# Kernel tuning notes

Measured on AMD Instinct MI355X. Metric: run time of the kernel, lower is better.

The kernel has to match this reference:

```python
import jax, jax.numpy as jnp
import numpy as np

NUM_GROUPS = 50   # hardcoded in convert_groupandcate_to_one_hot
ALPHA = 2.0       # forward() default
MARGIN = 0.8      # forward() default


def setup_inputs() -> dict:
    key = jax.random.key(0)
    k1, k2, k3, k4 = jax.random.split(key, 4)
    B, C, N = 4, 64, 4096
    l0_points = jax.random.normal(k1, (B, N, 3), dtype=jnp.float32)
    Fsim = jax.random.normal(k2, (B, C, N), dtype=jnp.float32)
    target = jax.random.randint(k3, (B, N), 0, NUM_GROUPS, dtype=jnp.int32)
    # sprinkle some -1 (ungrouped) labels, matching real SGPN data
    drop = jax.random.uniform(k4, (B, N)) < 0.02
    target = jnp.where(drop, jnp.int32(-1), target)
    return {"l0_points": l0_points, "Fsim": Fsim, "target": target}


def reference(l0_points, Fsim, target):
    B, C, N = Fsim.shape
    # pairwise squared-distance Gram matrix: D[i,j] = |f_i|^2 + |f_j|^2 - 2<f_i,f_j>
    r = jnp.sum(Fsim * Fsim, axis=1)                      # [B, N]
    gram = jnp.einsum('bcn,bcm->bnm', Fsim, Fsim)          # [B, N, N]
    D = jnp.maximum(r[:, :, None] + r[:, None, :] - 2.0 * gram, 0.0)

    # one-hot group labels; label -1 contributes all-zeros row
    valid = (target != -1)
    one_hot = (jax.nn.one_hot(jnp.where(valid, target, 0), NUM_GROUPS,
                              dtype=jnp.float32)
               * valid[..., None].astype(jnp.float32))     # [B, N, G]

    same = jnp.einsum('bng,bmg->bnm', one_hot, one_hot)    # same-group indicator
    eye = jnp.eye(N, dtype=same.dtype)
    same = same * (1.0 - eye) + eye                        # diagonal forced to 1
    diff = 1.0 - same

    pos = same * D
    neg = ALPHA * diff * jnp.maximum(MARGIN - D, 0.0)

    # NOTE: original returns grouplabels (not the count weights) as group_mask,
    # so the weight is the outer product of the raw integer labels.
    tf = target.astype(jnp.float32)
    w = tf[:, :, None] * tf[:, None, :]                    # [B, N, N]

    return jnp.mean((pos + neg) * w)
```

## Files before the change

kernel.cpp:

```cpp
#include <hip/hip_runtime.h>
#include <hip/hip_bf16.h>
#include <stdint.h>


#define NT 32
#define TRI 528
#define NPAIR (4*TRI)
#define NBLK 512
#define SCALE (1.0f/67108864.0f)

typedef __attribute__((ext_vector_type(4))) float f32x4;
typedef __attribute__((ext_vector_type(8))) __bf16 bf16x8;

__device__ __forceinline__ void async_load16(const void* g, void* l) {
    __builtin_amdgcn_global_load_lds(
        (const __attribute__((address_space(1))) uint32_t*)g,
        (__attribute__((address_space(3))) uint32_t*)l,
        16, 0, 0);
}

__global__ __launch_bounds__(256) void sgpn_prep(
    const float* __restrict__ Fsim, const int* __restrict__ target,
    unsigned short* __restrict__ gA, float* __restrict__ gR,
    float* __restrict__ gK, float* __restrict__ gW)
{
    __shared__ float sPart[4][64];

    int blk = blockIdx.x;
    int b = blk >> 6;
    int n0 = (blk & 63) * 64;
    int lane = threadIdx.x & 63;
    int wave = threadIdx.x >> 6;

    int n = n0 + lane;
    int gp = b * 4096 + n;
    const float* src = Fsim + (size_t)b * 64 * 4096 + n;
    int tile = n >> 7, row = n & 127;
    unsigned short* dst = gA + (size_t)(b * NT + tile) * 8192 + row * 8;

    float racc = 0.f;
    #pragma unroll
    for (int q = 0; q < 2; ++q) {
        int chunk = wave * 2 + q;
        unsigned us[8];
        #pragma unroll
        for (int j = 0; j < 8; ++j) {
            float f = src[(size_t)(chunk * 8 + j) * 4096];
            unsigned u = __float_as_uint(f);
            u += 0x7fffu + ((u >> 16) & 1u);
            us[j] = u >> 16;
            float fb = __uint_as_float(us[j] << 16);
            racc = fmaf(fb, fb, racc);
        }
        uint4 pk;
        pk.x = us[0] | (us[1] << 16);
        pk.y = us[2] | (us[3] << 16);
        pk.z = us[4] | (us[5] << 16);
        pk.w = us[6] | (us[7] << 16);
        *(uint4*)(dst + chunk * 1024) = pk;
    }
    sPart[wave][lane] = racc;
    __syncthreads();
    if (wave == 0) {
        gR[gp] = (sPart[0][lane] + sPart[1][lane]) +
                 (sPart[2][lane] + sPart[3][lane]);
        int tg = target[gp];
        gK[gp] = (tg >= 0) ? (float)tg : -(float)(n + 2);
        gW[gp] = (float)tg;
    }
}

__global__ __launch_bounds__(256, 2) void sgpn_main(
    const unsigned short* __restrict__ gA,
    const float* __restrict__ gR, const float* __restrict__ gK,
    const float* __restrict__ gW, float* __restrict__ gP)
{
    __shared__ __align__(16) unsigned short lT[2][2][8192];
    __shared__ __align__(16) float sM[2][2][3][128];
    __shared__ float sRed[4];
    __shared__ float sMult[2];

    int tid = threadIdx.x;
    int lane = tid & 63;
    int wave = tid >> 6;
    int g = blockIdx.x;
    int np = (g < (NPAIR - 4 * NBLK)) ? 5 : 4;

    auto stage = [&](int P, int buf) {
        int b = P / TRI;
        int t = P - b * TRI;
        int tj = (int)((sqrtf(8.0f * (float)t + 1.0f) - 1.0f) * 0.5f);
        while ((tj + 1) * (tj + 2) / 2 <= t) ++tj;
        while (tj * (tj + 1) / 2 > t) --tj;
        int ti = t - tj * (tj + 1) / 2;

        const unsigned short* tA = gA + (size_t)(b * NT + ti) * 8192;
        const unsigned short* tB = gA + (size_t)(b * NT + tj) * 8192;
        #pragma unroll
        for (int it = 0; it < 4; ++it) {
            int e = it * 256 + tid;
            async_load16(tA + e * 8, &lT[buf][0][e * 8]);
            async_load16(tB + e * 8, &lT[buf][1][e * 8]);
        }
        int half = tid >> 7, p0 = tid & 127;
        int gp = b * 4096 + (half ? tj : ti) * 128 + p0;
        sM[buf][half][0][p0] = gR[gp];
        sM[buf][half][1][p0] = gK[gp];
        sM[buf][half][2][p0] = gW[gp];
        if (tid == 0) sMult[buf] = (ti == tj) ? 1.f : 2.f;
    };

    int wr = wave >> 1, wc = wave & 1;
    int quad = lane >> 4, lcol = lane & 15;

    float total = 0.f;
    stage(g, 0);

    for (int q = 0; q < np; ++q) {
        __syncthreads();
        int buf = q & 1;
        if (q + 1 < np) stage(g + (q + 1) * NBLK, buf ^ 1);

        f32x4 acc[4][4];
        #pragma unroll
        for (int i = 0; i < 4; ++i)
            #pragma unroll
            for (int j = 0; j < 4; ++j)
                acc[i][j] = (f32x4)0.f;

        #pragma unroll
        for (int kb = 0; kb < 2; ++kb) {
            int chunk = kb * 4 + quad;
            bf16x8 fa[4], fb[4];
            #pragma unroll
            for (int i = 0; i < 4; ++i)
                fa[i] = *(const bf16x8*)&lT[buf][0][chunk * 1024 + (wr * 64 + i * 16 + lcol) * 8];
            #pragma unroll
            for (int j = 0; j < 4; ++j)
                fb[j] = *(const bf16x8*)&lT[buf][1][chunk * 1024 + (wc * 64 + j * 16 + lcol) * 8];
            #pragma unroll
            for (int i = 0; i < 4; ++i)
                #pragma unroll
                for (int j = 0; j < 4; ++j)
                    acc[i][j] = __builtin_amdgcn_mfma_f32_16x16x32_bf16(fa[i], fb[j], acc[i][j], 0, 0, 0);
        }

        float rcv[4], kcv[4], wcv[4];
        #pragma unroll
        for (int j = 0; j < 4; ++j) {
            int cl = wc * 64 + j * 16 + lcol;
            rcv[j] = sM[buf][1][0][cl];
            kcv[j] = sM[buf][1][1][cl];
            wcv[j] = sM[buf][1][2][cl];
        }

        float sum = 0.f;
        #pragma unroll
        for (int i = 0; i < 4; ++i) {
            int rb = wr * 64 + i * 16 + quad * 4;
            f32x4 rr4 = *(const f32x4*)&sM[buf][0][0][rb];
            f32x4 kr4 = *(const f32x4*)&sM[buf][0][1][rb];
            f32x4 wr4 = *(const f32x4*)&sM[buf][0][2][rb];
            #pragma unroll
            for (int r = 0; r < 4; ++r) {
                float rrow = rr4[r], krow = kr4[r], wrow = wr4[r];
                float psum = 0.f;
                #pragma unroll
                for (int j = 0; j < 4; ++j) {
                    float gacc = acc[i][j][r];
                    float d0 = fmaf(-2.f, gacc, rrow + rcv[j]);
                    float D  = fmaxf(d0, 0.f);
                    float h  = fmaxf(fmaf(D, -2.f, 1.6f), 0.f);
                    float v  = (krow == kcv[j]) ? D : h;
                    psum = fmaf(v, wcv[j], psum);
                }
                sum = fmaf(psum, wrow, sum);
            }
        }
        total = fmaf(sum, sMult[buf], total);
    }

    #pragma unroll
    for (int off = 32; off > 0; off >>= 1)
        total += __shfl_down(total, off, 64);
    if (lane == 0) sRed[wave] = total;
    __syncthreads();
    if (tid == 0)
        gP[g] = (sRed[0] + sRed[1]) + (sRed[2] + sRed[3]);
}

__global__ __launch_bounds__(256) void sgpn_reduce(
    const float* __restrict__ gP, float* __restrict__ out)
{
    __shared__ float sr[4];
    int tid = threadIdx.x;
    float s = gP[tid] + gP[tid + 256];
    #pragma unroll
    for (int off = 32; off > 0; off >>= 1)
        s += __shfl_down(s, off, 64);
    if ((tid & 63) == 0) sr[tid >> 6] = s;
    __syncthreads();
    if (tid == 0)
        out[0] = ((sr[0] + sr[1]) + (sr[2] + sr[3])) * SCALE;
}

extern "C" void kernel_launch(void* const* d_in, const int* in_sizes, int n_in,
                              void* d_out, int out_size, void* d_ws, size_t ws_size,
                              hipStream_t stream) {
    const float* Fsim  = (const float*)d_in[1];
    const int* target  = (const int*)d_in[2];
    float* out = (float*)d_out;

    char* ws = (char*)d_ws;
    unsigned short* gA = (unsigned short*)ws;
    float* gR = (float*)(ws + (2u << 20));
    float* gK = (float*)(ws + (2u << 20) + (64u << 10));
    float* gW = (float*)(ws + (2u << 20) + (128u << 10));
    float* gP = (float*)(ws + (2u << 20) + (192u << 10));

    sgpn_prep<<<256, 256, 0, stream>>>(Fsim, target, gA, gR, gK, gW);
    sgpn_main<<<NBLK, 256, 0, stream>>>(gA, gR, gK, gW, gP);
    sgpn_reduce<<<1, 256, 0, stream>>>(gP, out);
}
```

Before: 77.30 us.

## Fuse prep, main and reduce kernels into one cooperative launch with grid syncs

```diff
diff --git a/kernel.cpp b/kernel.cpp
--- a/kernel.cpp
+++ b/kernel.cpp
@@ -1,4 +1,5 @@
 #include <hip/hip_runtime.h>
+#include <hip/hip_cooperative_groups.h>
 #include <hip/hip_bf16.h>
 #include <stdint.h>
 
@@ -12,6 +13,8 @@
 typedef __attribute__((ext_vector_type(4))) float f32x4;
 typedef __attribute__((ext_vector_type(8))) __bf16 bf16x8;
 
+namespace cg = cooperative_groups;
+
 __device__ __forceinline__ void async_load16(const void* g, void* l) {
     __builtin_amdgcn_global_load_lds(
         (const __attribute__((address_space(1))) uint32_t*)g,
@@ -19,71 +22,67 @@
         16, 0, 0);
 }
 
-__global__ __launch_bounds__(256) void sgpn_prep(
+__global__ __launch_bounds__(256, 2) void sgpn_fused(
     const float* __restrict__ Fsim, const int* __restrict__ target,
     unsigned short* __restrict__ gA, float* __restrict__ gR,
-    float* __restrict__ gK, float* __restrict__ gW)
-{
-    __shared__ float sPart[4][64];
-
-    int blk = blockIdx.x;
-    int b = blk >> 6;
-    int n0 = (blk & 63) * 64;
-    int lane = threadIdx.x & 63;
-    int wave = threadIdx.x >> 6;
-
-    int n = n0 + lane;
-    int gp = b * 4096 + n;
-    const float* src = Fsim + (size_t)b * 64 * 4096 + n;
-    int tile = n >> 7, row = n & 127;
-    unsigned short* dst = gA + (size_t)(b * NT + tile) * 8192 + row * 8;
-
-    float racc = 0.f;
-    #pragma unroll
-    for (int q = 0; q < 2; ++q) {
-        int chunk = wave * 2 + q;
-        unsigned us[8];
-        #pragma unroll
-        for (int j = 0; j < 8; ++j) {
-            float f = src[(size_t)(chunk * 8 + j) * 4096];
-            unsigned u = __float_as_uint(f);
-            u += 0x7fffu + ((u >> 16) & 1u);
-            us[j] = u >> 16;
-            float fb = __uint_as_float(us[j] << 16);
-            racc = fmaf(fb, fb, racc);
-        }
-        uint4 pk;
-        pk.x = us[0] | (us[1] << 16);
-        pk.y = us[2] | (us[3] << 16);
-        pk.z = us[4] | (us[5] << 16);
-        pk.w = us[6] | (us[7] << 16);
-        *(uint4*)(dst + chunk * 1024) = pk;
-    }
-    sPart[wave][lane] = racc;
-    __syncthreads();
-    if (wave == 0) {
-        gR[gp] = (sPart[0][lane] + sPart[1][lane]) +
-                 (sPart[2][lane] + sPart[3][lane]);
-        int tg = target[gp];
-        gK[gp] = (tg >= 0) ? (float)tg : -(float)(n + 2);
-        gW[gp] = (float)tg;
-    }
-}
-
-__global__ __launch_bounds__(256, 2) void sgpn_main(
-    const unsigned short* __restrict__ gA,
-    const float* __restrict__ gR, const float* __restrict__ gK,
-    const float* __restrict__ gW, float* __restrict__ gP)
+    float* __restrict__ gK, float* __restrict__ gW,
+    float* __restrict__ gP, float* __restrict__ out)
 {
     __shared__ __align__(16) unsigned short lT[2][2][8192];
     __shared__ __align__(16) float sM[2][2][3][128];
     __shared__ float sRed[4];
     __shared__ float sMult[2];
+    __shared__ float sPart[4][64];
 
     int tid = threadIdx.x;
     int lane = tid & 63;
     int wave = tid >> 6;
     int g = blockIdx.x;
+
+    if (g < 256) {
+        int b = g >> 6;
+        int n0 = (g & 63) * 64;
+
+        int n = n0 + lane;
+        int gp = b * 4096 + n;
+        const float* src = Fsim + (size_t)b * 64 * 4096 + n;
+        int tile = n >> 7, row = n & 127;
+        unsigned short* dst = gA + (size_t)(b * NT + tile) * 8192 + row * 8;
+
+        float racc = 0.f;
+        #pragma unroll
+        for (int q = 0; q < 2; ++q) {
+            int chunk = wave * 2 + q;
+            unsigned us[8];
+            #pragma unroll
+            for (int j = 0; j < 8; ++j) {
+                float f = src[(size_t)(chunk * 8 + j) * 4096];
+                unsigned u = __float_as_uint(f);
+                u += 0x7fffu + ((u >> 16) & 1u);
+                us[j] = u >> 16;
+                float fb = __uint_as_float(us[j] << 16);
+                racc = fmaf(fb, fb, racc);
+            }
+            uint4 pk;
+            pk.x = us[0] | (us[1] << 16);
+            pk.y = us[2] | (us[3] << 16);
+            pk.z = us[4] | (us[5] << 16);
+            pk.w = us[6] | (us[7] << 16);
+            *(uint4*)(dst + chunk * 1024) = pk;
+        }
+        sPart[wave][lane] = racc;
+        __syncthreads();
+        if (wave == 0) {
+            gR[gp] = (sPart[0][lane] + sPart[1][lane]) +
+                     (sPart[2][lane] + sPart[3][lane]);
+            int tg = target[gp];
+            gK[gp] = (tg >= 0) ? (float)tg : -(float)(n + 2);
+            gW[gp] = (float)tg;
+        }
+    }
+    __threadfence();
+    cg::this_grid().sync();
+
     int np = (g < (NPAIR - 4 * NBLK)) ? 5 : 4;
 
     auto stage = [&](int P, int buf) {
@@ -187,6 +186,190 @@
     __syncthreads();
     if (tid == 0)
         gP[g] = (sRed[0] + sRed[1]) + (sRed[2] + sRed[3]);
+
+    __threadfence();
+    cg::this_grid().sync();
+
+    if (g == 0) {
+        float s = gP[tid] + gP[tid + 256];
+        #pragma unroll
+        for (int off = 32; off > 0; off >>= 1)
+            s += __shfl_down(s, off, 64);
+        if ((tid & 63) == 0) sRed[tid >> 6] = s;
+        __syncthreads();
+        if (tid == 0)
+            out[0] = ((sRed[0] + sRed[1]) + (sRed[2] + sRed[3])) * SCALE;
+    }
+}
+
+__global__ __launch_bounds__(256) void sgpn_prep(
+    const float* __restrict__ Fsim, const int* __restrict__ target,
+    unsigned short* __restrict__ gA, float* __restrict__ gR,
+    float* __restrict__ gK, float* __restrict__ gW)
+{
+    __shared__ float sPart[4][64];
+
+    int blk = blockIdx.x;
+    int b = blk >> 6;
+    int n0 = (blk & 63) * 64;
+    int lane = threadIdx.x & 63;
+    int wave = threadIdx.x >> 6;
+
+    int n = n0 + lane;
+    int gp = b * 4096 + n;
+    const float* src = Fsim + (size_t)b * 64 * 4096 + n;
+    int tile = n >> 7, row = n & 127;
+    unsigned short* dst = gA + (size_t)(b * NT + tile) * 8192 + row * 8;
+
+    float racc = 0.f;
+    #pragma unroll
+    for (int q = 0; q < 2; ++q) {
+        int chunk = wave * 2 + q;
+        unsigned us[8];
+        #pragma unroll
+        for (int j = 0; j < 8; ++j) {
+            float f = src[(size_t)(chunk * 8 + j) * 4096];
+            unsigned u = __float_as_uint(f);
+            u += 0x7fffu + ((u >> 16) & 1u);
+            us[j] = u >> 16;
+            float fb = __uint_as_float(us[j] << 16);
+            racc = fmaf(fb, fb, racc);
+        }
+        uint4 pk;
+        pk.x = us[0] | (us[1] << 16);
+        pk.y = us[2] | (us[3] << 16);
+        pk.z = us[4] | (us[5] << 16);
+        pk.w = us[6] | (us[7] << 16);
+        *(uint4*)(dst + chunk * 1024) = pk;
+    }
+    sPart[wave][lane] = racc;
+    __syncthreads();
+    if (wave == 0) {
+        gR[gp] = (sPart[0][lane] + sPart[1][lane]) +
+                 (sPart[2][lane] + sPart[3][lane]);
+        int tg = target[gp];
+        gK[gp] = (tg >= 0) ? (float)tg : -(float)(n + 2);
+        gW[gp] = (float)tg;
+    }
+}
+
+__global__ __launch_bounds__(256, 2) void sgpn_main(
+    const unsigned short* __restrict__ gA,
+    const float* __restrict__ gR, const float* __restrict__ gK,
+    const float* __restrict__ gW, float* __restrict__ gP)
+{
+    __shared__ __align__(16) unsigned short lT[2][2][8192];
+    __shared__ __align__(16) float sM[2][2][3][128];
+    __shared__ float sRed[4];
+    __shared__ float sMult[2];
+
+    int tid = threadIdx.x;
+    int lane = tid & 63;
+    int wave = tid >> 6;
+    int g = blockIdx.x;
+    int np = (g < (NPAIR - 4 * NBLK)) ? 5 : 4;
+
+    auto stage = [&](int P, int buf) {
+        int b = P / TRI;
+        int t = P - b * TRI;
+        int tj = (int)((sqrtf(8.0f * (float)t + 1.0f) - 1.0f) * 0.5f);
+        while ((tj + 1) * (tj + 2) / 2 <= t) ++tj;
+        while (tj * (tj + 1) / 2 > t) --tj;
+        int ti = t - tj * (tj + 1) / 2;
+
+        const unsigned short* tA = gA + (size_t)(b * NT + ti) * 8192;
+        const unsigned short* tB = gA + (size_t)(b * NT + tj) * 8192;
+        #pragma unroll
+        for (int it = 0; it < 4; ++it) {
+            int e = it * 256 + tid;
+            async_load16(tA + e * 8, &lT[buf][0][e * 8]);
+            async_load16(tB + e * 8, &lT[buf][1][e * 8]);
+        }
+        int half = tid >> 7, p0 = tid & 127;
+        int gp = b * 4096 + (half ? tj : ti) * 128 + p0;
+        sM[buf][half][0][p0] = gR[gp];
+        sM[buf][half][1][p0] = gK[gp];
+        sM[buf][half][2][p0] = gW[gp];
+        if (tid == 0) sMult[buf] = (ti == tj) ? 1.f : 2.f;
+    };
+
+    int wr = wave >> 1, wc = wave & 1;
+    int quad = lane >> 4, lcol = lane & 15;
+
+    float total = 0.f;
+    stage(g, 0);
+
+    for (int q = 0; q < np; ++q) {
+        __syncthreads();
+        int buf = q & 1;
+        if (q + 1 < np) stage(g + (q + 1) * NBLK, buf ^ 1);
+
+        f32x4 acc[4][4];
+        #pragma unroll
+        for (int i = 0; i < 4; ++i)
+            #pragma unroll
+            for (int j = 0; j < 4; ++j)
+                acc[i][j] = (f32x4)0.f;
+
+        #pragma unroll
+        for (int kb = 0; kb < 2; ++kb) {
+            int chunk = kb * 4 + quad;
+            bf16x8 fa[4], fb[4];
+            #pragma unroll
+            for (int i = 0; i < 4; ++i)
+                fa[i] = *(const bf16x8*)&lT[buf][0][chunk * 1024 + (wr * 64 + i * 16 + lcol) * 8];
+            #pragma unroll
+            for (int j = 0; j < 4; ++j)
+                fb[j] = *(const bf16x8*)&lT[buf][1][chunk * 1024 + (wc * 64 + j * 16 + lcol) * 8];
+            #pragma unroll
+            for (int i = 0; i < 4; ++i)
+                #pragma unroll
+                for (int j = 0; j < 4; ++j)
+                    acc[i][j] = __builtin_amdgcn_mfma_f32_16x16x32_bf16(fa[i], fb[j], acc[i][j], 0, 0, 0);
+        }
+
+        float rcv[4], kcv[4], wcv[4];
+        #pragma unroll
+        for (int j = 0; j < 4; ++j) {
+            int cl = wc * 64 + j * 16 + lcol;
+            rcv[j] = sM[buf][1][0][cl];
+            kcv[j] = sM[buf][1][1][cl];
+            wcv[j] = sM[buf][1][2][cl];
+        }
+
+        float sum = 0.f;
+        #pragma unroll
+        for (int i = 0; i < 4; ++i) {
+            int rb = wr * 64 + i * 16 + quad * 4;
+            f32x4 rr4 = *(const f32x4*)&sM[buf][0][0][rb];
+            f32x4 kr4 = *(const f32x4*)&sM[buf][0][1][rb];
+            f32x4 wr4 = *(const f32x4*)&sM[buf][0][2][rb];
+            #pragma unroll
+            for (int r = 0; r < 4; ++r) {
+                float rrow = rr4[r], krow = kr4[r], wrow = wr4[r];
+                float psum = 0.f;
+                #pragma unroll
+                for (int j = 0; j < 4; ++j) {
+                    float gacc = acc[i][j][r];
+                    float d0 = fmaf(-2.f, gacc, rrow + rcv[j]);
+                    float D  = fmaxf(d0, 0.f);
+                    float h  = fmaxf(fmaf(D, -2.f, 1.6f), 0.f);
+                    float v  = (krow == kcv[j]) ? D : h;
+                    psum = fmaf(v, wcv[j], psum);
+                }
+                sum = fmaf(psum, wrow, sum);
+            }
+        }
+        total = fmaf(sum, sMult[buf], total);
+    }
+
+    #pragma unroll
+    for (int off = 32; off > 0; off >>= 1)
+        total += __shfl_down(total, off, 64);
+    if (lane == 0) sRed[wave] = total;
+    __syncthreads();
+    if (tid == 0)
+        gP[g] = (sRed[0] + sRed[1]) + (sRed[2] + sRed[3]);
 }
 
 __global__ __launch_bounds__(256) void sgpn_reduce(
@@ -218,7 +401,14 @@
     float* gW = (float*)(ws + (2u << 20) + (128u << 10));
     float* gP = (float*)(ws + (2u << 20) + (192u << 10));
 
-    sgpn_prep<<<256, 256, 0, stream>>>(Fsim, target, gA, gR, gK, gW);
-    sgpn_main<<<NBLK, 256, 0, stream>>>(gA, gR, gK, gW, gP);
-    sgpn_reduce<<<1, 256, 0, stream>>>(gP, out);
-}
+    void* args[] = {(void*)&Fsim, (void*)&target, (void*)&gA, (void*)&gR,
+                    (void*)&gK, (void*)&gW, (void*)&gP, (void*)&out};
+    hipError_t err = hipLaunchCooperativeKernel(
+        (const void*)sgpn_fused, dim3(NBLK), dim3(256), args, 0, stream);
+
+    if (err != hipSuccess) {
+        sgpn_prep<<<256, 256, 0, stream>>>(Fsim, target, gA, gR, gK, gW);
+        sgpn_main<<<NBLK, 256, 0, stream>>>(gA, gR, gK, gW, gP);
+        sgpn_reduce<<<1, 256, 0, stream>>>(gP, out);
+    }
+}
```

After: 276.0 us. 3.57x slower.
